# Kernel optimization log

Hardware: AMD Instinct MI355X
Metric: run time of the kernel (lower is better)

Reference implementation:

```python
import jax, jax.numpy as jnp
import numpy as np
import math

N = 50000   # nodes
E = 800000  # edges
D = 64      # in_feat_dim == out_feat_dim
T = 8       # num node types
R = 8       # num relations
SQRT_DK = math.sqrt(D)


def typed_matmul(x, W, types, num_types):
    """Row-wise x[i] @ W[types[i]] without materializing [E, D, D] gathered weights."""
    out = jnp.zeros((x.shape[0], W.shape[-1]), x.dtype)
    for t in range(num_types):
        out = out + jnp.where((types == t)[:, None], x @ W[t], 0.0)
    return out


def segment_softmax(score, index, num_segments):
    smax = jax.ops.segment_max(score, index, num_segments=num_segments)
    ex = jnp.exp(score - smax[index])
    ssum = jax.ops.segment_sum(ex, index, num_segments=num_segments)
    return ex / (ssum[index] + 1e-16)


def setup_inputs() -> dict:
    key = jax.random.key(0)
    ks = jax.random.split(key, 10)
    h = jax.random.normal(ks[0], (N, D), dtype=jnp.float32)
    adj = jax.random.randint(ks[1], (2, E), 0, N, dtype=jnp.int64)
    edge_type = jax.random.randint(ks[2], (E,), 0, R, dtype=jnp.int64)
    node_type = jax.random.randint(ks[3], (N,), 0, T, dtype=jnp.int64)
    k_weights = jax.random.uniform(ks[4], (T, D, D), dtype=jnp.float32)
    q_weights = jax.random.uniform(ks[5], (T, D, D), dtype=jnp.float32)
    v_weights = jax.random.uniform(ks[6], (T, D, D), dtype=jnp.float32)
    a_weights = jax.random.uniform(ks[7], (T, D, D), dtype=jnp.float32)
    relation_att = jax.random.uniform(ks[8], (R, D, D), dtype=jnp.float32)
    relation_msg = jax.random.uniform(ks[9], (R, D, D), dtype=jnp.float32)
    relation_pri = jnp.ones((R, 1), dtype=jnp.float32)
    skip = jnp.ones((T,), dtype=jnp.float32)
    return {
        "h": h, "adj": adj, "edge_type": edge_type, "node_type": node_type,
        "src_type": 0, "dst_type": 0,
        "k_weights": k_weights, "q_weights": q_weights, "v_weights": v_weights,
        "a_weights": a_weights, "relation_pri": relation_pri,
        "relation_att": relation_att, "relation_msg": relation_msg, "skip": skip,
    }


def reference(h, adj, edge_type, node_type, src_type, dst_type,
              k_weights, q_weights, v_weights, a_weights,
              relation_pri, relation_att, relation_msg, skip):
    src = adj[0]  # _j side (messages come from src)
    dst = adj[1]  # _i side (scatter/softmax index)

    # Node-type-indexed projections (done per node, then gathered per edge --
    # identical math to the per-edge bmm in the original).
    k_node = typed_matmul(h, k_weights, node_type, T)  # [N, D]
    q_node = typed_matmul(h, q_weights, node_type, T)
    v_node = typed_matmul(h, v_weights, node_type, T)

    # Relation-indexed per-edge transforms.
    k = typed_matmul(k_node[src], relation_att, edge_type, R)  # [E, D]
    v = typed_matmul(v_node[src], relation_msg, edge_type, R)  # [E, D]
    q = q_node[dst]                                            # [E, D]

    attn_score = jnp.sum(k * q, axis=1, keepdims=True) * relation_pri[edge_type] / SQRT_DK  # [E, 1]
    alpha = segment_softmax(attn_score, dst, N)  # edge softmax over incoming edges
    rst = v * alpha                              # [E, D]

    agg = jax.ops.segment_sum(rst, dst, num_segments=N)  # [N, D]

    # Update: node-type-indexed output transform scaled by sigmoid(skip[type]).
    trans_out = typed_matmul(agg, a_weights, node_type, T)
    alpha_skip = jax.nn.sigmoid(skip[node_type])
    return trans_out * alpha_skip[:, None]
```

## Files before the change

kernel.cpp:

```cpp
#include <hip/hip_runtime.h>
#include <math.h>

typedef float f32x4 __attribute__((ext_vector_type(4)));
typedef short bf16x8 __attribute__((ext_vector_type(8)));
typedef _Float16 f16x8 __attribute__((ext_vector_type(8)));
typedef _Float16 f16x4 __attribute__((ext_vector_type(4)));

#define D 64
#define TT 8
#define RR 8

#define SCAN_TPB 256
#define SCAN_CH 4
#define SCAN_ELEMS (SCAN_TPB * SCAN_CH)

#define HIST_CH 8
#define SCAT_CH 4
#define SCORE_BX 1024

__device__ __forceinline__ float bf2f(unsigned short u) {
    union { unsigned int i; float f; } x;
    x.i = ((unsigned int)u) << 16;
    return x.f;
}
__device__ __forceinline__ unsigned short f2bf(float f) {
    union { float f; unsigned int i; } x;
    x.f = f;
    unsigned int i = x.i;
    unsigned int r = (i + 0x7FFFu + ((i >> 16) & 1u)) >> 16;
    return (unsigned short)r;
}
struct BfPair { short hi; short lo; };
__device__ __forceinline__ BfPair split2(float x) {
    BfPair p;
    unsigned short h = f2bf(x);
    p.hi = (short)h;
    p.lo = (short)f2bf(x - bf2f(h));
    return p;
}
__device__ __forceinline__ void load_A_split(const float* __restrict__ p, bf16x8& ah, bf16x8& al) {
#pragma unroll
    for (int i = 0; i < 8; ++i) {
        BfPair s = split2(p[i]);
        ah[i] = s.hi; al[i] = s.lo;
    }
}
__device__ __forceinline__ void load_B_split(const float* __restrict__ W, int ks, int c, int lane,
                                             bf16x8& bh, bf16x8& bl) {
    int n = lane & 15, q = lane >> 4;
#pragma unroll
    for (int i = 0; i < 8; ++i) {
        BfPair s = split2(W[(ks * 32 + q * 8 + i) * 64 + c * 16 + n]);
        bh[i] = s.hi; bl[i] = s.lo;
    }
}
__device__ __forceinline__ void load_B_split_f16(const float* __restrict__ W, int ks, int c, int lane,
                                                 f16x8& bh, f16x8& bl) {
    int n = lane & 15, q = lane >> 4;
#pragma unroll
    for (int i = 0; i < 8; ++i) {
        float w = W[(ks * 32 + q * 8 + i) * 64 + c * 16 + n];
        _Float16 h = (_Float16)w;
        bh[i] = h;
        bl[i] = (_Float16)(w - (float)h);
    }
}
__device__ __forceinline__ f16x8 load_B_frag_f16(const float* __restrict__ W, int ks, int c, int lane) {
    int n = lane & 15, q = lane >> 4;
    f16x8 r;
#pragma unroll
    for (int i = 0; i < 8; ++i)
        r[i] = (_Float16)W[(ks * 32 + q * 8 + i) * 64 + c * 16 + n];
    return r;
}

#define MFMA16(a, b, c) __builtin_amdgcn_mfma_f32_16x16x32_bf16(a, b, c, 0, 0, 0)
#define MFMAH(a, b, c)  __builtin_amdgcn_mfma_f32_16x16x32_f16(a, b, c, 0, 0, 0)

#define SPLIT_MFMA_BODY(acc, A0h, A0l, A1h, A1l, Bh, Bl)          \
    _Pragma("unroll")                                             \
    for (int c = 0; c < 4; ++c) {                                 \
        acc[c] = MFMA16(A0h, Bh[0][c], acc[c]);                   \
        acc[c] = MFMA16(A0l, Bh[0][c], acc[c]);                   \
        acc[c] = MFMA16(A0h, Bl[0][c], acc[c]);                   \
        acc[c] = MFMA16(A1h, Bh[1][c], acc[c]);                   \
        acc[c] = MFMA16(A1l, Bh[1][c], acc[c]);                   \
        acc[c] = MFMA16(A1h, Bl[1][c], acc[c]);                   \
    }

__global__ void hist_kernel(const int* __restrict__ dst, const int* __restrict__ et,
                            const int* __restrict__ nt,
                            int* __restrict__ deg, int* __restrict__ tcnt, int* __restrict__ rcnt,
                            int* __restrict__ erank, int N, int E) {
    __shared__ int l_r[RR], l_t[TT];
    if (threadIdx.x < RR) l_r[threadIdx.x] = 0;
    if (threadIdx.x < TT) l_t[threadIdx.x] = 0;
    __syncthreads();
    const int stride = gridDim.x * blockDim.x;
    const int tid = blockIdx.x * blockDim.x + threadIdx.x;
#pragma unroll
    for (int i = 0; i < HIST_CH; ++i) {
        int e = tid + i * stride;
        if (e < E) {
            erank[e] = atomicAdd(&deg[dst[e]], 1);
            atomicAdd(&l_r[et[e]], 1);
        }
    }
#pragma unroll
    for (int i = 0; i < HIST_CH; ++i) {
        int n = tid + i * stride;
        if (n < N) atomicAdd(&l_t[nt[n]], 1);
    }
    __syncthreads();
    if (threadIdx.x < RR && l_r[threadIdx.x]) atomicAdd(&rcnt[threadIdx.x], l_r[threadIdx.x]);
    if (threadIdx.x < TT && l_t[threadIdx.x]) atomicAdd(&tcnt[threadIdx.x], l_t[threadIdx.x]);
}

__global__ void scan_sum_kernel(const int* __restrict__ deg, int* __restrict__ bsum, int N) {
    __shared__ int ws[SCAN_TPB / 64];
    int tid = threadIdx.x;
    int base = blockIdx.x * SCAN_ELEMS + tid * SCAN_CH;
    int s = 0;
#pragma unroll
    for (int i = 0; i < SCAN_CH; ++i) {
        int idx = base + i;
        if (idx < N) s += deg[idx];
    }
#pragma unroll
    for (int d = 32; d; d >>= 1) s += __shfl_xor(s, d, 64);
    if ((tid & 63) == 0) ws[tid >> 6] = s;
    __syncthreads();
    if (tid == 0) {
        int t = 0;
#pragma unroll
        for (int i = 0; i < SCAN_TPB / 64; ++i) t += ws[i];
        bsum[blockIdx.x] = t;
    }
}
__global__ void scan_out_kernel(const int* __restrict__ deg, const int* __restrict__ bsum, int nsb,
                                int* __restrict__ off, int N, int Etot,
                                const int* __restrict__ tcnt, int* __restrict__ toff, int* __restrict__ tcur,
                                const int* __restrict__ rcnt, int* __restrict__ roff, int* __restrict__ rcur) {
    __shared__ int ts[SCAN_TPB];
    __shared__ int bb;
    int tid = threadIdx.x;
    if (tid < 64) {
        int v = 0;
        if (nsb <= 64) {
            v = (tid < nsb && tid < blockIdx.x) ? bsum[tid] : 0;
#pragma unroll
            for (int d = 32; d; d >>= 1) v += __shfl_xor(v, d, 64);
        } else if (tid == 0) {
            for (int b = 0; b < blockIdx.x; ++b) v += bsum[b];
        }
        if (tid == 0) bb = v;
    }
    if (blockIdx.x == 0 && tid == 1) {
        int a = 0;
        for (int t = 0; t < TT; ++t) { toff[t] = a; tcur[t] = a; a += tcnt[t]; }
        toff[TT] = a;
        int b2 = 0;
        for (int r = 0; r < RR; ++r) { roff[r] = b2; rcur[r] = b2; b2 += rcnt[r]; }
        roff[RR] = b2;
        off[N] = Etot;
    }
    int base = blockIdx.x * SCAN_ELEMS + tid * SCAN_CH;
    int loc[SCAN_CH];
    int s = 0;
#pragma unroll
    for (int i = 0; i < SCAN_CH; ++i) {
        int idx = base + i;
        int v = (idx < N) ? deg[idx] : 0;
        loc[i] = v; s += v;
    }
    ts[tid] = s;
    __syncthreads();
    for (int sh = 1; sh < SCAN_TPB; sh <<= 1) {
        int v = (tid >= sh) ? ts[tid - sh] : 0;
        __syncthreads();
        ts[tid] += v;
        __syncthreads();
    }
    int run = bb + ((tid > 0) ? ts[tid - 1] : 0);
#pragma unroll
    for (int i = 0; i < SCAN_CH; ++i) {
        int idx = base + i;
        if (idx < N) { off[idx] = run; run += loc[i]; }
    }
}

__global__ void scatter_kernel(const int* __restrict__ src, const int* __restrict__ dst,
                               const int* __restrict__ et, const int* __restrict__ nt,
                               const int* __restrict__ offs, const int* __restrict__ erank,
                               int* __restrict__ tcur, int* __restrict__ rcur,
                               int* __restrict__ rsrc, int* __restrict__ rdst,
                               int* __restrict__ rdpos, int* __restrict__ nidx, int N, int E) {
    __shared__ int l_r[RR], l_t[TT], base_r[RR], base_t[TT];
    if (threadIdx.x < RR) l_r[threadIdx.x] = 0;
    if (threadIdx.x < TT) l_t[threadIdx.x] = 0;
    __syncthreads();
    const int stride = gridDim.x * blockDim.x;
    const int tid = blockIdx.x * blockDim.x + threadIdx.x;
    int s[SCAT_CH], d[SCAT_CH], r[SCAT_CH], rrank[SCAT_CH];
    int t[SCAT_CH], trank[SCAT_CH];
#pragma unroll
    for (int i = 0; i < SCAT_CH; ++i) {
        int e = tid + i * stride;
        if (e < E) {
            s[i] = src[e]; d[i] = dst[e]; r[i] = et[e];
            rrank[i] = atomicAdd(&l_r[r[i]], 1);
        }
        int n = tid + i * stride;
        if (n < N) {
            t[i] = nt[n];
            trank[i] = atomicAdd(&l_t[t[i]], 1);
        }
    }
    __syncthreads();
    if (threadIdx.x < RR)
        base_r[threadIdx.x] = l_r[threadIdx.x] ? atomicAdd(&rcur[threadIdx.x], l_r[threadIdx.x]) : 0;
    if (threadIdx.x < TT)
        base_t[threadIdx.x] = l_t[threadIdx.x] ? atomicAdd(&tcur[threadIdx.x], l_t[threadIdx.x]) : 0;
    __syncthreads();
#pragma unroll
    for (int i = 0; i < SCAT_CH; ++i) {
        int e = tid + i * stride;
        if (e < E) {
            int pos = offs[d[i]] + erank[e];
            int rp = base_r[r[i]] + rrank[i];
            rsrc[rp] = s[i]; rdst[rp] = d[i]; rdpos[rp] = pos;
        }
        int n = tid + i * stride;
        if (n < N) nidx[base_t[t[i]] + trank[i]] = n;
    }
}

__global__ void proj_kernel(const float* __restrict__ h,
                            const float* __restrict__ Wk, const float* __restrict__ Wq,
                            const float* __restrict__ Wv,
                            const int* __restrict__ toff, const int* __restrict__ nidx,
                            _Float16* __restrict__ kh16,
                            _Float16* __restrict__ qout, _Float16* __restrict__ vout) {
    const int t = blockIdx.z, a = blockIdx.y, lane = threadIdx.x;
    const int beg = toff[t], end = toff[t + 1], cnt = end - beg;
    if (cnt <= 0) return;
    const int nstrips = (cnt + 15) >> 4;
    const float* W = (a == 0 ? Wk : (a == 1 ? Wq : Wv)) + (size_t)t * 4096;
    const int m = lane & 15, quad = lane >> 4;

    bf16x8 Bh[2][4], Bl[2][4];
#pragma unroll
    for (int ks = 0; ks < 2; ++ks)
#pragma unroll
        for (int c = 0; c < 4; ++c) load_B_split(W, ks, c, lane, Bh[ks][c], Bl[ks][c]);

    _Float16* out = (a == 0) ? kh16 : (a == 1 ? qout : vout);

    for (int s = blockIdx.x; s < nstrips; s += gridDim.x) {
        int base = beg + s * 16;
        int rA = base + m; if (rA > end - 1) rA = end - 1;
        const float* hp = h + (size_t)nidx[rA] * D;
        bf16x8 A0h, A0l, A1h, A1l;
        load_A_split(hp + quad * 8, A0h, A0l);
        load_A_split(hp + 32 + quad * 8, A1h, A1l);
        f32x4 acc[4];
#pragma unroll
        for (int c = 0; c < 4; ++c) acc[c] = (f32x4){0.f, 0.f, 0.f, 0.f};
        SPLIT_MFMA_BODY(acc, A0h, A0l, A1h, A1l, Bh, Bl)
#pragma unroll
        for (int reg = 0; reg < 4; ++reg) {
            int rr = base + quad * 4 + reg;
            if (rr < end) {
                int nid = nidx[rr];
#pragma unroll
                for (int c = 0; c < 4; ++c)
                    out[(size_t)nid * D + c * 16 + m] = (_Float16)acc[c][reg];
            }
        }
    }
}

__global__ void score_v2_kernel(const int* __restrict__ rsrc, const int* __restrict__ rdst,
                                const int* __restrict__ rdpos, const int* __restrict__ roff,
                                const _Float16* __restrict__ kh16,
                                const _Float16* __restrict__ qn, const float* __restrict__ Aatt,
                                const float* __restrict__ pri, int2* __restrict__ rec,
                                const _Float16* __restrict__ vn, const float* __restrict__ Amsg,
                                _Float16* __restrict__ V2, int N) {
    const int r = blockIdx.y, lane = threadIdx.x;
    const int m = lane & 15, quad = lane >> 4;

    if (blockIdx.x >= SCORE_BX) {
        const int bx = blockIdx.x - SCORE_BX;
        const int gx = gridDim.x - SCORE_BX;
        const int nstrips = (N + 15) >> 4;
        const float* W = Amsg + (size_t)r * 4096;
        f16x8 B[2][4];
#pragma unroll
        for (int ks = 0; ks < 2; ++ks)
#pragma unroll
            for (int c = 0; c < 4; ++c) B[ks][c] = load_B_frag_f16(W, ks, c, lane);

        for (int s = bx; s < nstrips; s += gx) {
            int base = s * 16;
            int rA = base + m; if (rA > N - 1) rA = N - 1;
            f16x8 A0 = *(const f16x8*)(vn + (size_t)rA * D + quad * 8);
            f16x8 A1 = *(const f16x8*)(vn + (size_t)rA * D + 32 + quad * 8);
            f32x4 acc[4];
#pragma unroll
            for (int c = 0; c < 4; ++c) acc[c] = (f32x4){0.f, 0.f, 0.f, 0.f};
#pragma unroll
            for (int c = 0; c < 4; ++c) {
                acc[c] = MFMAH(A0, B[0][c], acc[c]);
                acc[c] = MFMAH(A1, B[1][c], acc[c]);
            }
#pragma unroll
            for (int reg = 0; reg < 4; ++reg) {
                int rr = base + quad * 4 + reg;
                if (rr < N) {
#pragma unroll
                    for (int c = 0; c < 4; ++c)
                        V2[((size_t)rr * RR + r) * D + c * 16 + m] = (_Float16)acc[c][reg];
                }
            }
        }
        return;
    }

    const int beg = roff[r], end = roff[r + 1], cnt = end - beg;
    if (cnt <= 0) return;
    const int nstrips = (cnt + 15) >> 4;
    const float scale = pri[r] * 0.125f;
    const float* W = Aatt + (size_t)r * 4096;

    f16x8 Bh[2][4], Bl[2][4];
#pragma unroll
    for (int ks = 0; ks < 2; ++ks)
#pragma unroll
        for (int c = 0; c < 4; ++c) load_B_split_f16(W, ks, c, lane, Bh[ks][c], Bl[ks][c]);

    for (int st = blockIdx.x; st < nstrips; st += SCORE_BX) {
        int base = st * 16;
        int ia = base + m; if (ia > cnt - 1) ia = cnt - 1;
        int s = rsrc[beg + ia];
        const _Float16* kr = kh16 + (size_t)s * D;
        f16x8 A0 = *(const f16x8*)(kr + quad * 8);
        f16x8 A1 = *(const f16x8*)(kr + 32 + quad * 8);
        f32x4 acc[4];
#pragma unroll
        for (int c = 0; c < 4; ++c) acc[c] = (f32x4){0.f, 0.f, 0.f, 0.f};
#pragma unroll
        for (int c = 0; c < 4; ++c) {
            acc[c] = MFMAH(A0, Bh[0][c], acc[c]);
            acc[c] = MFMAH(A0, Bl[0][c], acc[c]);
            acc[c] = MFMAH(A1, Bh[1][c], acc[c]);
            acc[c] = MFMAH(A1, Bl[1][c], acc[c]);
        }

        float p4[4];
#pragma unroll
        for (int reg = 0; reg < 4; ++reg) {
            int ie = base + quad * 4 + reg; if (ie > cnt - 1) ie = cnt - 1;
            const _Float16* qp = qn + (size_t)rdst[beg + ie] * D + m;
            float pr = acc[0][reg] * (float)qp[0] + acc[1][reg] * (float)qp[16]
                     + acc[2][reg] * (float)qp[32] + acc[3][reg] * (float)qp[48];
#pragma unroll
            for (int d = 8; d; d >>= 1) pr += __shfl_xor(pr, d, 64);
            p4[reg] = pr;
        }
        if (m < 4) {
            int idx = base + quad * 4 + m;
            if (idx < cnt) {
                float v = (m == 0) ? p4[0] : (m == 1) ? p4[1] : (m == 2) ? p4[2] : p4[3];
                int sagain = rsrc[beg + idx];
                int2 rc;
                rc.x = __float_as_int(v * scale);
                rc.y = (sagain << 3) | r;
                rec[rdpos[beg + idx]] = rc;
            }
        }
    }
}

__global__ void agg_kernel(const int* __restrict__ offs, const int2* __restrict__ rec,
                           const _Float16* __restrict__ V2,
                           float* __restrict__ agg, int N) {
    const int lane = threadIdx.x & 63;
    const int wv = threadIdx.x >> 6;
    const int quad = lane >> 4, ql = lane & 15;
    const int i = blockIdx.x * 16 + wv * 4 + quad;
    if (i >= N) return;
    const int beg = offs[i], end = offs[i + 1];
    const int qb = quad << 4;
    float mmax = -INFINITY, lsum = 0.f;
    float a0 = 0.f, a1 = 0.f, a2 = 0.f, a3 = 0.f;
    for (int cs = beg; cs < end; cs += 16) {
        int cl = end - cs; if (cl > 16) cl = 16;
        int2 rc; rc.y = 0;
        float sc = -INFINITY;
        if (ql < cl) { rc = rec[cs + ql]; sc = __int_as_float(rc.x); }
        float cm = sc;
#pragma unroll
        for (int d = 8; d; d >>= 1) cm = fmaxf(cm, __shfl_xor(cm, d, 64));
        float mn = fmaxf(mmax, cm);
        float cf = __expf(mmax - mn);
        float ex = (ql < cl) ? __expf(sc - mn) : 0.f;
        float csum = ex;
#pragma unroll
        for (int d = 8; d; d >>= 1) csum += __shfl_xor(csum, d, 64);
        lsum = lsum * cf + csum;
        a0 *= cf; a1 *= cf; a2 *= cf; a3 *= cf;
        for (int e = 0; e < cl; e += 4) {
            float w0 = __shfl(ex, qb + e, 64),     w1 = __shfl(ex, qb + e + 1, 64);
            float w2 = __shfl(ex, qb + e + 2, 64), w3 = __shfl(ex, qb + e + 3, 64);
            int   i0 = __shfl(rc.y, qb + e, 64),     i1 = __shfl(rc.y, qb + e + 1, 64);
            int   i2 = __shfl(rc.y, qb + e + 2, 64), i3 = __shfl(rc.y, qb + e + 3, 64);
            f16x4 v0 = *(const f16x4*)(V2 + (size_t)i0 * D + ql * 4);
            f16x4 v1 = *(const f16x4*)(V2 + (size_t)i1 * D + ql * 4);
            f16x4 v2 = *(const f16x4*)(V2 + (size_t)i2 * D + ql * 4);
            f16x4 v3 = *(const f16x4*)(V2 + (size_t)i3 * D + ql * 4);
            a0 += w0 * (float)v0[0] + w1 * (float)v1[0] + w2 * (float)v2[0] + w3 * (float)v3[0];
            a1 += w0 * (float)v0[1] + w1 * (float)v1[1] + w2 * (float)v2[1] + w3 * (float)v3[1];
            a2 += w0 * (float)v0[2] + w1 * (float)v1[2] + w2 * (float)v2[2] + w3 * (float)v3[2];
            a3 += w0 * (float)v0[3] + w1 * (float)v1[3] + w2 * (float)v2[3] + w3 * (float)v3[3];
        }
        mmax = mn;
    }
    float inv = 1.f / (lsum + 1e-16f);
    f32x4 outv = (f32x4){a0 * inv, a1 * inv, a2 * inv, a3 * inv};
    *(f32x4*)(agg + (size_t)i * D + ql * 4) = outv;
}

__global__ void out_kernel(float* __restrict__ io, const float* __restrict__ Wa,
                           const float* __restrict__ skip,
                           const int* __restrict__ toff, const int* __restrict__ nidx) {
    const int t = blockIdx.y, lane = threadIdx.x;
    const int beg = toff[t], end = toff[t + 1], cnt = end - beg;
    if (cnt <= 0) return;
    const int nstrips = (cnt + 15) >> 4;
    const float* W = Wa + (size_t)t * 4096;
    const float sg = 1.f / (1.f + __expf(-skip[t]));
    const int m = lane & 15, quad = lane >> 4;

    bf16x8 Bh[2][4], Bl[2][4];
#pragma unroll
    for (int ks = 0; ks < 2; ++ks)
#pragma unroll
        for (int c = 0; c < 4; ++c) load_B_split(W, ks, c, lane, Bh[ks][c], Bl[ks][c]);

    for (int s = blockIdx.x; s < nstrips; s += gridDim.x) {
        int base = beg + s * 16;
        int rA = base + m; if (rA > end - 1) rA = end - 1;
        const float* ap = io + (size_t)nidx[rA] * D;
        bf16x8 A0h, A0l, A1h, A1l;
        load_A_split(ap + quad * 8, A0h, A0l);
        load_A_split(ap + 32 + quad * 8, A1h, A1l);
        f32x4 acc[4];
#pragma unroll
        for (int c = 0; c < 4; ++c) acc[c] = (f32x4){0.f, 0.f, 0.f, 0.f};
        SPLIT_MFMA_BODY(acc, A0h, A0l, A1h, A1l, Bh, Bl)
#pragma unroll
        for (int reg = 0; reg < 4; ++reg) {
            int rr = base + quad * 4 + reg;
            if (rr < end) {
                size_t nb = (size_t)nidx[rr] * D;
#pragma unroll
                for (int c = 0; c < 4; ++c)
                    io[nb + c * 16 + m] = acc[c][reg] * sg;
            }
        }
    }
}

extern "C" void kernel_launch(void* const* d_in, const int* in_sizes, int n_in,
                              void* d_out, int out_size, void* d_ws, size_t ws_size,
                              hipStream_t stream) {
    const float* h     = (const float*)d_in[0];
    const int*   adj   = (const int*)d_in[1];
    const int*   etype = (const int*)d_in[2];
    const int*   ntype = (const int*)d_in[3];
    const float* Wk    = (const float*)d_in[6];
    const float* Wq    = (const float*)d_in[7];
    const float* Wv    = (const float*)d_in[8];
    const float* Wa    = (const float*)d_in[9];
    const float* pri   = (const float*)d_in[10];
    const float* Aatt  = (const float*)d_in[11];
    const float* Amsg  = (const float*)d_in[12];
    const float* skp   = (const float*)d_in[13];
    const int N = in_sizes[3];
    const int E = in_sizes[2];
    float* out = (float*)d_out;

    char* w = (char*)d_ws;
    auto alloc = [&](size_t b) { char* p = w; w += (b + 255) & ~(size_t)255; return p; };
    _Float16* kh16 = (_Float16*)alloc((size_t)N * D * 2);
    _Float16* qn   = (_Float16*)alloc((size_t)N * D * 2);
    _Float16* vn   = (_Float16*)alloc((size_t)N * D * 2);
    _Float16* V2   = (_Float16*)alloc((size_t)N * RR * D * 2);
    int* deg  = (int*)alloc((size_t)(N + 16) * 4);
    int* tcnt = deg + N;
    int* rcnt = deg + N + 8;
    int* offs = (int*)alloc((size_t)(N + 1) * 4);
    int* erank = (int*)alloc((size_t)E * 4);
    int* toff = (int*)alloc(64);
    int* tcur = (int*)alloc(64);
    int* roff = (int*)alloc(64);
    int* rcur = (int*)alloc(64);
    int2* rec = (int2*)alloc((size_t)E * 8);
    int* rsrc  = (int*)alloc((size_t)E * 4);
    int* rdst  = (int*)alloc((size_t)E * 4);
    int* rdpos = (int*)alloc((size_t)E * 4);
    int* nidx  = (int*)alloc((size_t)N * 4);
    const int nsb = (N + SCAN_ELEMS - 1) / SCAN_ELEMS;
    int* bsum  = (int*)alloc((size_t)nsb * 4);

    (void)hipMemsetAsync(deg, 0, (size_t)(N + 16) * 4, stream);

    const int mx = (E > N ? E : N);
    const int histBlocks = (mx + 256 * HIST_CH - 1) / (256 * HIST_CH);
    hist_kernel<<<histBlocks, 256, 0, stream>>>(adj + E, etype, ntype, deg, tcnt, rcnt, erank, N, E);
    scan_sum_kernel<<<nsb, SCAN_TPB, 0, stream>>>(deg, bsum, N);
    scan_out_kernel<<<nsb, SCAN_TPB, 0, stream>>>(deg, bsum, nsb, offs, N, E,
                                                  tcnt, toff, tcur, rcnt, roff, rcur);
    const int scatBlocks = (mx + 256 * SCAT_CH - 1) / (256 * SCAT_CH);
    scatter_kernel<<<scatBlocks, 256, 0, stream>>>(adj, adj + E, etype, ntype,
                                                   offs, erank, tcur, rcur,
                                                   rsrc, rdst, rdpos, nidx, N, E);
    proj_kernel<<<dim3(128, 3, TT), 64, 0, stream>>>(h, Wk, Wq, Wv, toff, nidx, kh16, qn, vn);
    score_v2_kernel<<<dim3(SCORE_BX + 256, RR), 64, 0, stream>>>(rsrc, rdst, rdpos, roff,
                                                                 kh16, qn, Aatt, pri, rec,
                                                                 vn, Amsg, V2, N);
    agg_kernel<<<(N + 15) / 16, 256, 0, stream>>>(offs, rec, V2, out, N);
    out_kernel<<<dim3(128, TT), 64, 0, stream>>>(out, Wa, skp, toff, nidx);
}
```

Before: 262.7 us.

## Fuse edge-softmax aggregation with output transform and widen score blocks

Merges the aggregation kernel and the typed output-projection kernel into one. Each block processes 16 nodes of one type, stages the aggregated rows in shared memory, and applies the split-bf16 MFMA with four waves, each covering 16 output columns. This drops the fp32 agg round-trip through global memory and one launch. The score/V2 kernel is also changed from 64-thread blocks to 256-thread blocks with four waves striding strips, using a smaller grid. In exchange, the fused kernel needs __syncthreads between the irregular per-node gather and the MFMA, so load imbalance across nodes within a block can stall the other waves.

```diff
diff --git a/kernel.cpp b/kernel.cpp
--- a/kernel.cpp
+++ b/kernel.cpp
@@ -16,7 +16,9 @@
 
 #define HIST_CH 8
 #define SCAT_CH 4
-#define SCORE_BX 1024
+#define SCORE_XB 256
+#define V2_XB 64
+#define AGG_XB 256
 
 __device__ __forceinline__ float bf2f(unsigned short u) {
     union { unsigned int i; float f; } x;
@@ -287,12 +289,13 @@
                                 const float* __restrict__ pri, int2* __restrict__ rec,
                                 const _Float16* __restrict__ vn, const float* __restrict__ Amsg,
                                 _Float16* __restrict__ V2, int N) {
-    const int r = blockIdx.y, lane = threadIdx.x;
+    const int r = blockIdx.y;
+    const int lane = threadIdx.x & 63;
+    const int wv = threadIdx.x >> 6;
     const int m = lane & 15, quad = lane >> 4;
 
-    if (blockIdx.x >= SCORE_BX) {
-        const int bx = blockIdx.x - SCORE_BX;
-        const int gx = gridDim.x - SCORE_BX;
+    if (blockIdx.x >= SCORE_XB) {
+        const int g = (blockIdx.x - SCORE_XB) * 4 + wv;
         const int nstrips = (N + 15) >> 4;
         const float* W = Amsg + (size_t)r * 4096;
         f16x8 B[2][4];
@@ -301,7 +304,7 @@
 #pragma unroll
             for (int c = 0; c < 4; ++c) B[ks][c] = load_B_frag_f16(W, ks, c, lane);
 
-        for (int s = bx; s < nstrips; s += gx) {
+        for (int s = g; s < nstrips; s += V2_XB * 4) {
             int base = s * 16;
             int rA = base + m; if (rA > N - 1) rA = N - 1;
             f16x8 A0 = *(const f16x8*)(vn + (size_t)rA * D + quad * 8);
@@ -339,7 +342,8 @@
 #pragma unroll
         for (int c = 0; c < 4; ++c) load_B_split_f16(W, ks, c, lane, Bh[ks][c], Bl[ks][c]);
 
-    for (int st = blockIdx.x; st < nstrips; st += SCORE_BX) {
+    const int g = blockIdx.x * 4 + wv;
+    for (int st = g; st < nstrips; st += SCORE_XB * 4) {
         int base = st * 16;
         int ia = base + m; if (ia > cnt - 1) ia = cnt - 1;
         int s = rsrc[beg + ia];
@@ -382,93 +386,93 @@
     }
 }
 
-__global__ void agg_kernel(const int* __restrict__ offs, const int2* __restrict__ rec,
-                           const _Float16* __restrict__ V2,
-                           float* __restrict__ agg, int N) {
+__global__ void agg_out_kernel(const int* __restrict__ offs, const int2* __restrict__ rec,
+                               const _Float16* __restrict__ V2,
+                               const float* __restrict__ Wa, const float* __restrict__ skp,
+                               const int* __restrict__ toff, const int* __restrict__ nidx,
+                               float* __restrict__ out) {
+    const int t = blockIdx.y;
+    const int beg = toff[t], end = toff[t + 1], cnt = end - beg;
+    if (cnt <= 0) return;
+    const int nstrips = (cnt + 15) >> 4;
     const int lane = threadIdx.x & 63;
     const int wv = threadIdx.x >> 6;
     const int quad = lane >> 4, ql = lane & 15;
-    const int i = blockIdx.x * 16 + wv * 4 + quad;
-    if (i >= N) return;
-    const int beg = offs[i], end = offs[i + 1];
+    const int q16 = wv * 4 + quad;
     const int qb = quad << 4;
-    float mmax = -INFINITY, lsum = 0.f;
-    float a0 = 0.f, a1 = 0.f, a2 = 0.f, a3 = 0.f;
-    for (int cs = beg; cs < end; cs += 16) {
-        int cl = end - cs; if (cl > 16) cl = 16;
-        int2 rc; rc.y = 0;
-        float sc = -INFINITY;
-        if (ql < cl) { rc = rec[cs + ql]; sc = __int_as_float(rc.x); }
-        float cm = sc;
-#pragma unroll
-        for (int d = 8; d; d >>= 1) cm = fmaxf(cm, __shfl_xor(cm, d, 64));
-        float mn = fmaxf(mmax, cm);
-        float cf = __expf(mmax - mn);
-        float ex = (ql < cl) ? __expf(sc - mn) : 0.f;
-        float csum = ex;
-#pragma unroll
-        for (int d = 8; d; d >>= 1) csum += __shfl_xor(csum, d, 64);
-        lsum = lsum * cf + csum;
-        a0 *= cf; a1 *= cf; a2 *= cf; a3 *= cf;
-        for (int e = 0; e < cl; e += 4) {
-            float w0 = __shfl(ex, qb + e, 64),     w1 = __shfl(ex, qb + e + 1, 64);
-            float w2 = __shfl(ex, qb + e + 2, 64), w3 = __shfl(ex, qb + e + 3, 64);
-            int   i0 = __shfl(rc.y, qb + e, 64),     i1 = __shfl(rc.y, qb + e + 1, 64);
-            int   i2 = __shfl(rc.y, qb + e + 2, 64), i3 = __shfl(rc.y, qb + e + 3, 64);
-            f16x4 v0 = *(const f16x4*)(V2 + (size_t)i0 * D + ql * 4);
-            f16x4 v1 = *(const f16x4*)(V2 + (size_t)i1 * D + ql * 4);
-            f16x4 v2 = *(const f16x4*)(V2 + (size_t)i2 * D + ql * 4);
-            f16x4 v3 = *(const f16x4*)(V2 + (size_t)i3 * D + ql * 4);
-            a0 += w0 * (float)v0[0] + w1 * (float)v1[0] + w2 * (float)v2[0] + w3 * (float)v3[0];
-            a1 += w0 * (float)v0[1] + w1 * (float)v1[1] + w2 * (float)v2[1] + w3 * (float)v3[1];
-            a2 += w0 * (float)v0[2] + w1 * (float)v1[2] + w2 * (float)v2[2] + w3 * (float)v3[2];
-            a3 += w0 * (float)v0[3] + w1 * (float)v1[3] + w2 * (float)v2[3] + w3 * (float)v3[3];
-        }
-        mmax = mn;
-    }
-    float inv = 1.f / (lsum + 1e-16f);
-    f32x4 outv = (f32x4){a0 * inv, a1 * inv, a2 * inv, a3 * inv};
-    *(f32x4*)(agg + (size_t)i * D + ql * 4) = outv;
-}
-
-__global__ void out_kernel(float* __restrict__ io, const float* __restrict__ Wa,
-                           const float* __restrict__ skip,
-                           const int* __restrict__ toff, const int* __restrict__ nidx) {
-    const int t = blockIdx.y, lane = threadIdx.x;
-    const int beg = toff[t], end = toff[t + 1], cnt = end - beg;
-    if (cnt <= 0) return;
-    const int nstrips = (cnt + 15) >> 4;
+    const int m = lane & 15, qd = lane >> 4;
+    const float sg = 1.f / (1.f + __expf(-skp[t]));
+
+    __shared__ float As[16][68];
+
+    bf16x8 Bh2[2], Bl2[2];
     const float* W = Wa + (size_t)t * 4096;
-    const float sg = 1.f / (1.f + __expf(-skip[t]));
-    const int m = lane & 15, quad = lane >> 4;
-
-    bf16x8 Bh[2][4], Bl[2][4];
-#pragma unroll
-    for (int ks = 0; ks < 2; ++ks)
-#pragma unroll
-        for (int c = 0; c < 4; ++c) load_B_split(W, ks, c, lane, Bh[ks][c], Bl[ks][c]);
+#pragma unroll
+    for (int ks = 0; ks < 2; ++ks) load_B_split(W, ks, wv, lane, Bh2[ks], Bl2[ks]);
 
     for (int s = blockIdx.x; s < nstrips; s += gridDim.x) {
         int base = beg + s * 16;
-        int rA = base + m; if (rA > end - 1) rA = end - 1;
-        const float* ap = io + (size_t)nidx[rA] * D;
+        int rr = base + q16; if (rr > end - 1) rr = end - 1;
+        int i = nidx[rr];
+        const int ebeg = offs[i], eend = offs[i + 1];
+        float mmax = -INFINITY, lsum = 0.f;
+        float a0 = 0.f, a1 = 0.f, a2 = 0.f, a3 = 0.f;
+        for (int cs = ebeg; cs < eend; cs += 16) {
+            int cl = eend - cs; if (cl > 16) cl = 16;
+            int2 rc; rc.y = 0;
+            float sc = -INFINITY;
+            if (ql < cl) { rc = rec[cs + ql]; sc = __int_as_float(rc.x); }
+            float cm = sc;
+#pragma unroll
+            for (int d = 8; d; d >>= 1) cm = fmaxf(cm, __shfl_xor(cm, d, 64));
+            float mn = fmaxf(mmax, cm);
+            float cf = __expf(mmax - mn);
+            float ex = (ql < cl) ? __expf(sc - mn) : 0.f;
+            float csum = ex;
+#pragma unroll
+            for (int d = 8; d; d >>= 1) csum += __shfl_xor(csum, d, 64);
+            lsum = lsum * cf + csum;
+            a0 *= cf; a1 *= cf; a2 *= cf; a3 *= cf;
+            for (int e = 0; e < cl; e += 4) {
+                float w0 = __shfl(ex, qb + e, 64),     w1 = __shfl(ex, qb + e + 1, 64);
+                float w2 = __shfl(ex, qb + e + 2, 64), w3 = __shfl(ex, qb + e + 3, 64);
+                int   i0 = __shfl(rc.y, qb + e, 64),     i1 = __shfl(rc.y, qb + e + 1, 64);
+                int   i2 = __shfl(rc.y, qb + e + 2, 64), i3 = __shfl(rc.y, qb + e + 3, 64);
+                f16x4 v0 = *(const f16x4*)(V2 + (size_t)i0 * D + ql * 4);
+                f16x4 v1 = *(const f16x4*)(V2 + (size_t)i1 * D + ql * 4);
+                f16x4 v2 = *(const f16x4*)(V2 + (size_t)i2 * D + ql * 4);
+                f16x4 v3 = *(const f16x4*)(V2 + (size_t)i3 * D + ql * 4);
+                a0 += w0 * (float)v0[0] + w1 * (float)v1[0] + w2 * (float)v2[0] + w3 * (float)v3[0];
+                a1 += w0 * (float)v0[1] + w1 * (float)v1[1] + w2 * (float)v2[1] + w3 * (float)v3[1];
+                a2 += w0 * (float)v0[2] + w1 * (float)v1[2] + w2 * (float)v2[2] + w3 * (float)v3[2];
+                a3 += w0 * (float)v0[3] + w1 * (float)v1[3] + w2 * (float)v2[3] + w3 * (float)v3[3];
+            }
+            mmax = mn;
+        }
+        float inv = 1.f / (lsum + 1e-16f);
+        As[q16][ql * 4 + 0] = a0 * inv;
+        As[q16][ql * 4 + 1] = a1 * inv;
+        As[q16][ql * 4 + 2] = a2 * inv;
+        As[q16][ql * 4 + 3] = a3 * inv;
+        __syncthreads();
+
         bf16x8 A0h, A0l, A1h, A1l;
-        load_A_split(ap + quad * 8, A0h, A0l);
-        load_A_split(ap + 32 + quad * 8, A1h, A1l);
-        f32x4 acc[4];
-#pragma unroll
-        for (int c = 0; c < 4; ++c) acc[c] = (f32x4){0.f, 0.f, 0.f, 0.f};
-        SPLIT_MFMA_BODY(acc, A0h, A0l, A1h, A1l, Bh, Bl)
+        load_A_split(&As[m][qd * 8], A0h, A0l);
+        load_A_split(&As[m][32 + qd * 8], A1h, A1l);
+        f32x4 acc = (f32x4){0.f, 0.f, 0.f, 0.f};
+        acc = MFMA16(A0h, Bh2[0], acc);
+        acc = MFMA16(A0l, Bh2[0], acc);
+        acc = MFMA16(A0h, Bl2[0], acc);
+        acc = MFMA16(A1h, Bh2[1], acc);
+        acc = MFMA16(A1l, Bh2[1], acc);
+        acc = MFMA16(A1h, Bl2[1], acc);
 #pragma unroll
         for (int reg = 0; reg < 4; ++reg) {
-            int rr = base + quad * 4 + reg;
-            if (rr < end) {
-                size_t nb = (size_t)nidx[rr] * D;
-#pragma unroll
-                for (int c = 0; c < 4; ++c)
-                    io[nb + c * 16 + m] = acc[c][reg] * sg;
-            }
-        }
+            int rrr = base + qd * 4 + reg;
+            if (rrr < end)
+                out[(size_t)nidx[rrr] * D + wv * 16 + m] = acc[reg] * sg;
+        }
+        __syncthreads();
     }
 }
 
@@ -527,9 +531,8 @@
                                                    offs, erank, tcur, rcur,
                                                    rsrc, rdst, rdpos, nidx, N, E);
     proj_kernel<<<dim3(128, 3, TT), 64, 0, stream>>>(h, Wk, Wq, Wv, toff, nidx, kh16, qn, vn);
-    score_v2_kernel<<<dim3(SCORE_BX + 256, RR), 64, 0, stream>>>(rsrc, rdst, rdpos, roff,
-                                                                 kh16, qn, Aatt, pri, rec,
-                                                                 vn, Amsg, V2, N);
-    agg_kernel<<<(N + 15) / 16, 256, 0, stream>>>(offs, rec, V2, out, N);
-    out_kernel<<<dim3(128, TT), 64, 0, stream>>>(out, Wa, skp, toff, nidx);
-}
+    score_v2_kernel<<<dim3(SCORE_XB + V2_XB, RR), 256, 0, stream>>>(rsrc, rdst, rdpos, roff,
+                                                                    kh16, qn, Aatt, pri, rec,
+                                                                    vn, Amsg, V2, N);
+    agg_out_kernel<<<dim3(AGG_XB, TT), 256, 0, stream>>>(offs, rec, V2, Wa, skp, toff, nidx, out);
+}
```

New measurement: 257.7 us. About the same (-1.9%).
